# Kernel optimization log

Measured on AMD Instinct MI355X. Metric: run time of the kernel, lower is better.

Reference implementation:

```python
import jax, jax.numpy as jnp
import numpy as np

HIDDEN = 384
NDIM = 3
N_POINTS = 100000
N_SUPER = 2048
MAX_DEG = 32
RADIUS = 0.045
INPUT_DIM = 3


def _sincos_embed(coords):
    # ContinuousSincosEmbed: dim=384, ndim=3 -> 128 channels per spatial dim (64 sin + 64 cos)
    eff = HIDDEN // NDIM  # 128
    omega = jnp.arange(0, eff, 2, dtype=jnp.float32) / eff
    freq = 1.0 / (10000.0 ** omega)  # [eff//2]
    out = coords[..., None] * freq  # [..., ndim, eff//2]
    emb = jnp.concatenate([jnp.sin(out), jnp.cos(out)], axis=-1)  # [..., ndim, eff]
    return emb.reshape(coords.shape[:-1] + (HIDDEN,))


def _radius_neighbors(pos, sn_idx):
    # numpy preprocessing equivalent of torch_geometric.nn.pool.radius with
    # max_num_neighbors=MAX_DEG; fixed-size padded [S, K] output + validity mask.
    nbr = np.zeros((N_SUPER, MAX_DEG), np.int32)
    mask = np.zeros((N_SUPER, MAX_DEG), bool)
    pos2 = (pos ** 2).sum(-1)
    r2 = RADIUS * RADIUS
    chunk = 128
    for i0 in range(0, N_SUPER, chunk):
        sp = pos[sn_idx[i0:i0 + chunk]]
        d2 = (sp ** 2).sum(-1)[:, None] + pos2[None, :] - 2.0 * (sp @ pos.T)
        within = d2 <= r2
        for j in range(sp.shape[0]):
            idx = np.nonzero(within[j])[0][:MAX_DEG]
            nbr[i0 + j, :len(idx)] = idx
            mask[i0 + j, :len(idx)] = True
    return nbr, mask


def setup_inputs() -> dict:
    rng = np.random.default_rng(0)
    pos = rng.random((N_POINTS, NDIM)).astype(np.float32)
    sn_idx = np.sort(rng.choice(N_POINTS, N_SUPER, replace=False)).astype(np.int32)
    nbr, mask = _radius_neighbors(pos, sn_idx)
    key = jax.random.key(0)
    ks = jax.random.split(key, 6)
    s = 0.02  # truncnormal002 init scale
    return {
        "input_pos": jnp.asarray(pos),
        "input_feat": jax.random.normal(ks[0], (N_POINTS, INPUT_DIM), jnp.float32),
        "supernode_idx": jnp.asarray(sn_idx),
        "neighbor_idx": jnp.asarray(nbr),
        "neighbor_mask": jnp.asarray(mask),
        "W_in": jax.random.normal(ks[1], (INPUT_DIM, HIDDEN), jnp.float32) * s,
        "b_in": jnp.zeros((HIDDEN,), jnp.float32),
        "W1": jax.random.normal(ks[2], (2 * HIDDEN, HIDDEN), jnp.float32) * s,
        "b1": jnp.zeros((HIDDEN,), jnp.float32),
        "W2": jax.random.normal(ks[3], (HIDDEN, HIDDEN), jnp.float32) * s,
        "b2": jnp.zeros((HIDDEN,), jnp.float32),
        "W_proj": jax.random.normal(ks[4], (2 * HIDDEN, HIDDEN), jnp.float32) * s,
        "b_proj": jnp.zeros((HIDDEN,), jnp.float32),
    }


def reference(input_pos, input_feat, supernode_idx, neighbor_idx, neighbor_mask,
              W_in, b_in, W1, b1, W2, b2, W_proj, b_proj):
    # point embeddings: continuous sincos pos embed + input feature projection
    x = _sincos_embed(input_pos) + input_feat @ W_in + b_in          # [N, D]
    sn = x[supernode_idx]                                            # [S, D] supernode pos embed
    src = x[neighbor_idx]                                            # [S, K, D] gathered neighbors
    dst = jnp.broadcast_to(sn[:, None, :], src.shape)                # [S, K, D]
    h = jnp.concatenate([src, dst], axis=-1)                         # [S, K, 2D]
    # message MLP (Linear -> GELU(exact) -> Linear), as nn.GELU default
    h = jax.nn.gelu(h @ W1 + b1, approximate=False) @ W2 + b2        # [S, K, D]
    # masked mean == segment_csr(..., reduce='mean') over variable-degree edges
    m = neighbor_mask[..., None].astype(h.dtype)
    agg = (h * m).sum(axis=1) / jnp.maximum(m.sum(axis=1), 1.0)      # [S, D]
    # readd_supernode_pos: concat supernode pos embed, project 2D -> D
    out = jnp.concatenate([agg, sn], axis=-1) @ W_proj + b_proj      # [S, D]
    return out[None]                                                 # [1, S, D] (batch_size=1)
```

## Files before the change

### kernel.cpp

```cpp
#include <hip/hip_runtime.h>
#include <hip/hip_bf16.h>
#include <cstdint>

#define HIDDEN 384
#define NSUPER 2048
#define WBLK  (12*24*64*8)

typedef __attribute__((ext_vector_type(8)))  short bf16x8;
typedef __attribute__((ext_vector_type(4)))  float f32x4;
typedef __attribute__((ext_vector_type(16))) float f32x16;

__device__ inline unsigned short f2bf(float f) {
    unsigned int u = __float_as_uint(f);
    return (unsigned short)((u + 0x7fffu + ((u >> 16) & 1u)) >> 16);
}
__device__ inline bf16x8 pack8(const float* v) {
    union { bf16x8 v8; unsigned short u[8]; } u;
    #pragma unroll
    for (int i = 0; i < 8; ++i) u.u[i] = f2bf(v[i]);
    return u.v8;
}
__device__ inline float gelu(float y) {
    const float y2 = y * y;
    const float m  = __expf(y * fmaf(-0.0713548163f, y2, -1.5957691216f));
    return y * (1.0f / (1.0f + m));
}

__global__ __launch_bounds__(256)
void prep(const float* __restrict__ W1, const float* __restrict__ W2,
          const float* __restrict__ Wp, const unsigned int* __restrict__ mask,
          const float* __restrict__ pos, const float* __restrict__ feat,
          const int* __restrict__ sn_idx,
          const float* __restrict__ W_in, const float* __restrict__ b_in,
          unsigned short* __restrict__ w1s32, unsigned short* __restrict__ w1df,
          unsigned short* __restrict__ w2f,  unsigned short* __restrict__ wpf,
          unsigned short* __restrict__ snxb, int* __restrict__ flag) {
    const int b = blockIdx.x;
    const int t = threadIdx.x;
    if (b == 360) {
        __shared__ int s;
        if (t == 0) s = 0;
        __syncthreads();
        int bad = 0;
        for (int i = t; i < 16384; i += 256)
            if (mask[i] > 1u) bad = 1;
        if (bad) s = 1;
        __syncthreads();
        if (t == 0) *flag = s;
        return;
    }
    if (b > 360) {
        __shared__ float W4[HIDDEN][4];
        __shared__ float P6[64][7];
        const int eb = b - 361;
        if (t < 64) {
            const int pi = sn_idx[eb*64 + t];
            P6[t][0]=pos[pi*3];  P6[t][1]=pos[pi*3+1];  P6[t][2]=pos[pi*3+2];
            P6[t][3]=feat[pi*3]; P6[t][4]=feat[pi*3+1]; P6[t][5]=feat[pi*3+2];
        }
        for (int d = t; d < HIDDEN; d += 256) {
            W4[d][0]=W_in[d]; W4[d][1]=W_in[HIDDEN+d];
            W4[d][2]=W_in[2*HIDDEN+d]; W4[d][3]=b_in[d];
        }
        __syncthreads();
        const int er = t >> 2, seg = t & 3;
        float frA[8], frB[8];
        #pragma unroll
        for (int i = 0; i < 8; ++i) {
            frA[i] = exp2f(-(float)(seg*8 + i)      * 0.2076205059304601f);
            frB[i] = exp2f(-(float)(32 + seg*8 + i) * 0.2076205059304601f);
        }
        const float f0 = P6[er][3], f1 = P6[er][4], f2 = P6[er][5];
        #pragma unroll
        for (int cc = 0; cc < 3; ++cc) {
            const float pc = P6[er][cc];
            float sL[8], sH[8], cL[8], cH[8];
            #pragma unroll
            for (int i = 0; i < 8; ++i) {
                const float aL = pc*frA[i], aH = pc*frB[i];
                sL[i]=__sinf(aL); sH[i]=__sinf(aH); cL[i]=__cosf(aL); cH[i]=__cosf(aH);
            }
            #pragma unroll
            for (int q = 0; q < 4; ++q) {
                const float* bb = (q==0)?sL:(q==1)?sH:(q==2)?cL:cH;
                const int blk = cc*4 + q;
                float v[8];
                #pragma unroll
                for (int i = 0; i < 8; ++i) {
                    const int dim = blk*32 + seg*8 + i;
                    const float4 wv = *(const float4*)W4[dim];
                    v[i] = fmaf(f0, wv.x, fmaf(f1, wv.y, fmaf(f2, wv.z, bb[i] + wv.w)));
                }
                *(bf16x8*)&snxb[(size_t)(eb*64 + er)*HIDDEN + blk*32 + seg*8] = pack8(v);
            }
        }
        return;
    }
    const int grp = b / 72, sub = b % 72;
    const int idx = sub * 256 + t;
    const int l   = idx & 63;
    const int frag= idx >> 6;
    const float* W; unsigned short* out;
    int col, k0;
    if (grp == 0) {
        W = W1; out = w1s32;
        const int nt = frag % 12, kt = frag / 12;
        col = nt*32 + (l & 31);
        k0  = kt*16 + (l >> 5)*8;
    } else {
        switch (grp) {
            case 1: W = W1 + 384*HIDDEN; out = w1df; break;
            case 2: W = W2;              out = w2f;  break;
            case 3: W = Wp;              out = wpf;  break;
            default:W = Wp + 384*HIDDEN; out = wpf + WBLK; break;
        }
        const int nt = frag % 24, kt = frag / 24;
        col = nt*16 + (l & 15);
        k0  = kt*32 + (l >> 4)*8;
    }
    unsigned int pk[4];
    #pragma unroll
    for (int j = 0; j < 4; ++j) {
        unsigned int lo = f2bf(W[(size_t)(k0 + 2*j)     * HIDDEN + col]);
        unsigned int hi = f2bf(W[(size_t)(k0 + 2*j + 1) * HIDDEN + col]);
        pk[j] = lo | (hi << 16);
    }
    *reinterpret_cast<uint4*>(&out[(size_t)idx * 8]) =
        *reinterpret_cast<const uint4*>(pk);
}

__global__ __launch_bounds__(256)
void k_dstv(const unsigned short* __restrict__ snxb,
            const unsigned short* __restrict__ w1df,
            const float* __restrict__ b1, float* __restrict__ dstv) {
    const int rg = blockIdx.x >> 2, cq = blockIdx.x & 3;
    const int t = threadIdx.x, w = t>>6, l = t&63, lg = l>>4, l15 = l&15;
    const int wgm = w>>1, wgn = w&1;
    const int r0 = rg*64 + wgm*32;
    const int ntb = cq*6 + wgn*3;
    f32x4 acc[2][3];
    #pragma unroll
    for (int mt=0; mt<2; ++mt)
        #pragma unroll
        for (int nt=0; nt<3; ++nt) acc[mt][nt] = (f32x4){0.f,0.f,0.f,0.f};
    #pragma unroll 2
    for (int kt = 0; kt < 12; ++kt) {
        bf16x8 a[2], bfr[3];
        const unsigned short* bpp = &w1df[((size_t)(kt*24 + ntb)*64 + l)*8];
        #pragma unroll
        for (int nt=0; nt<3; ++nt) bfr[nt] = *(const bf16x8*)(bpp + (size_t)nt*512);
        #pragma unroll
        for (int mt=0; mt<2; ++mt)
            a[mt] = *(const bf16x8*)&snxb[(size_t)(r0 + mt*16 + l15)*HIDDEN + kt*32 + lg*8];
        #pragma unroll
        for (int mt=0; mt<2; ++mt)
            #pragma unroll
            for (int nt=0; nt<3; ++nt)
                acc[mt][nt] = __builtin_amdgcn_mfma_f32_16x16x32_bf16(a[mt], bfr[nt], acc[mt][nt], 0,0,0);
    }
    #pragma unroll
    for (int mt=0; mt<2; ++mt)
        #pragma unroll
        for (int nt=0; nt<3; ++nt) {
            const int col = cq*96 + wgn*48 + nt*16 + l15;
            #pragma unroll
            for (int r=0; r<4; ++r) {
                const int row = r0 + mt*16 + lg*4 + r;
                dstv[(size_t)row*HIDDEN + col] = acc[mt][nt][r] + b1[col];
            }
        }
}

__global__ __launch_bounds__(1024)
void k_mlp(const float* __restrict__ pos, const float* __restrict__ feat,
           const int* __restrict__ nbr_idx, const void* __restrict__ mask_raw,
           const int* __restrict__ mask_fmt,
           const float* __restrict__ W_in, const float* __restrict__ b_in,
           const float* __restrict__ dstv,
           const unsigned short* __restrict__ W1s32,
           unsigned short* __restrict__ aggpre, float* __restrict__ cntf)
{
    __shared__ unsigned short G[4*24*64*8];
    __shared__ float WIN0[HIDDEN], WIN1[HIDDEN], WIN2[HIDDEN], WINB[HIDDEN];
    __shared__ float PF[128][7];
    __shared__ float CNT[4];

    const int t  = threadIdx.x;
    const int bm = blockIdx.x;
    const int l = t & 63, w = t >> 6;
    const int mg = w >> 2, ng = w & 3;

    if (t < 128) {
        const int e  = bm*128 + t;
        const int pi = nbr_idx[e];
        PF[t][0]=pos[pi*3];  PF[t][1]=pos[pi*3+1];  PF[t][2]=pos[pi*3+2];
        PF[t][3]=feat[pi*3]; PF[t][4]=feat[pi*3+1]; PF[t][5]=feat[pi*3+2];
        const int fmt = *mask_fmt;
        const int mv  = fmt ? (int)((const unsigned char*)mask_raw)[e]
                            : ((const int*)mask_raw)[e];
        PF[t][6] = mv ? 1.0f : 0.0f;
    } else if (t >= 128 && t < 128 + HIDDEN) {
        const int d = t - 128;
        WIN0[d] = W_in[d];          WIN1[d] = W_in[HIDDEN + d];
        WIN2[d] = W_in[2*HIDDEN+d]; WINB[d] = b_in[d];
    }
    __syncthreads();
    if (t < 4) {
        float c = 0.f;
        for (int s = 0; s < 32; ++s) c += PF[t*32+s][6];
        CNT[t] = c;
    }

    {
        const int er = t >> 3, seg = t & 7;
        float frS[8];
        #pragma unroll
        for (int j = 0; j < 8; ++j)
            frS[j] = exp2f(-(float)(seg*8 + j) * 0.2076205059304601f);
        const float f0 = PF[er][3], f1 = PF[er][4], f2 = PF[er][5];
        const float pcs[3] = {PF[er][0], PF[er][1], PF[er][2]};
        const int lane = 32*(seg&1) + (er&31);
        const int ktb  = seg >> 1;
        const int mtb  = (er>>5)*24;
        #pragma unroll
        for (int cc = 0; cc < 3; ++cc) {
            const float pc = pcs[cc];
            #pragma unroll
            for (int sc = 0; sc < 2; ++sc) {
                const int kt = cc*8 + sc*4 + ktb;
                float v[8];
                #pragma unroll
                for (int j = 0; j < 8; ++j) {
                    const int dim = cc*128 + sc*64 + seg*8 + j;
                    const float aa = pc * frS[j];
                    const float base = sc ? __cosf(aa) : __sinf(aa);
                    v[j] = fmaf(f0, WIN0[dim], fmaf(f1, WIN1[dim],
                           fmaf(f2, WIN2[dim], base + WINB[dim])));
                }
                *(bf16x8*)&G[(size_t)((mtb + kt)*64 + lane)*8] = pack8(v);
            }
        }
    }
    __syncthreads();

    f32x16 acc[3];
    #pragma unroll
    for (int nt = 0; nt < 3; ++nt)
        #pragma unroll
        for (int r = 0; r < 16; ++r) acc[nt][r] = 0.f;

    bf16x8 bA[3], bB[3], aA, aB;
    #define LOADB(dst, kt)                                                       \
        { const unsigned short* bp_ = &W1s32[((size_t)((kt)*12 + ng*3)*64 + l)*8];\
          _Pragma("unroll")                                                      \
          for (int nt_ = 0; nt_ < 3; ++nt_)                                      \
              dst[nt_] = *(const bf16x8*)(bp_ + (size_t)nt_*512); }
    #define AREAD(kt) (*(const bf16x8*)&G[(size_t)((mg*24 + (kt))*64 + l)*8])
    #define MFMA3(bfr, a_)                                                       \
        { __builtin_amdgcn_s_setprio(1);                                         \
          _Pragma("unroll")                                                      \
          for (int nt_ = 0; nt_ < 3; ++nt_)                                      \
              acc[nt_] = __builtin_amdgcn_mfma_f32_32x32x16_bf16(                \
                  a_, bfr[nt_], acc[nt_], 0, 0, 0);                              \
          __builtin_amdgcn_s_setprio(0); }

    LOADB(bA, 0); LOADB(bB, 1);
    aA = AREAD(0); aB = AREAD(1);
    #pragma unroll
    for (int kt = 0; kt < 24; kt += 2) {
        MFMA3(bA, aA);
        if (kt + 2 < 24) { LOADB(bA, kt + 2); aA = AREAD(kt + 2); }
        MFMA3(bB, aB);
        if (kt + 3 < 24) { LOADB(bB, kt + 3); aB = AREAD(kt + 3); }
    }
    #undef LOADB
    #undef AREAD
    #undef MFMA3

    const int lh = l >> 5, l31 = l & 31;
    const int sn = bm*4 + mg;
    float dv[3];
    #pragma unroll
    for (int nt = 0; nt < 3; ++nt)
        dv[nt] = dstv[(size_t)sn*HIDDEN + ng*96 + nt*32 + l31];
    float mvr[16];
    #pragma unroll
    for (int r = 0; r < 16; ++r) {
        const int row = (r & 3) + 8*(r >> 2) + 4*lh;
        mvr[r] = PF[mg*32 + row][6];
    }
    const float inv = 1.0f / fmaxf(CNT[mg], 1.f);
    #pragma unroll
    for (int nt = 0; nt < 3; ++nt) {
        float s = 0.f;
        #pragma unroll
        for (int r = 0; r < 16; ++r)
            s += mvr[r] * gelu(acc[nt][r] + dv[nt]);
        s += __shfl_xor(s, 32);
        if (lh == 0)
            aggpre[(size_t)sn*HIDDEN + ng*96 + nt*32 + l31] = f2bf(s * inv);
    }
    if (t < 4) cntf[bm*4 + t] = CNT[t];
}

__global__ __launch_bounds__(256)
void k_out(const unsigned short* __restrict__ aggpre,
           const unsigned short* __restrict__ snxb,
           const unsigned short* __restrict__ w2f,
           const unsigned short* __restrict__ wpf,
           const float* __restrict__ b2, const float* __restrict__ bp,
           const float* __restrict__ cntf, float* __restrict__ out) {
    __shared__ unsigned short AGG[64][392];
    const int rg = blockIdx.x >> 2, cq = blockIdx.x & 3;
    const int t = threadIdx.x, w = t>>6, l = t&63, lg = l>>4, l15 = l&15;
    const int wgm = w>>1, wgn = w&1;
    const int r0g = rg*64;
    {
        const int rowm = wgm*32;
        f32x4 acc[2][12];
        #pragma unroll
        for (int mt=0; mt<2; ++mt)
            #pragma unroll
            for (int nt=0; nt<12; ++nt) acc[mt][nt] = (f32x4){0.f,0.f,0.f,0.f};
        for (int kt = 0; kt < 12; ++kt) {
            bf16x8 a[2], bfr[12];
            const unsigned short* bpp = &w2f[((size_t)(kt*24 + wgn*12)*64 + l)*8];
            #pragma unroll
            for (int nt=0; nt<12; ++nt) bfr[nt] = *(const bf16x8*)(bpp + (size_t)nt*512);
            #pragma unroll
            for (int mt=0; mt<2; ++mt)
                a[mt] = *(const bf16x8*)&aggpre[(size_t)(r0g + rowm + mt*16 + l15)*HIDDEN + kt*32 + lg*8];
            #pragma unroll
            for (int mt=0; mt<2; ++mt)
                #pragma unroll
                for (int nt=0; nt<12; ++nt)
                    acc[mt][nt] = __builtin_amdgcn_mfma_f32_16x16x32_bf16(a[mt], bfr[nt], acc[mt][nt], 0,0,0);
        }
        #pragma unroll
        for (int mt=0; mt<2; ++mt)
            #pragma unroll
            for (int nt=0; nt<12; ++nt) {
                const int col = wgn*192 + nt*16 + l15;
                const float bb = b2[col];
                #pragma unroll
                for (int r=0; r<4; ++r) {
                    const int row = rowm + mt*16 + lg*4 + r;
                    const float nz = (cntf[r0g + row] > 0.f) ? 1.f : 0.f;
                    AGG[row][col] = f2bf(acc[mt][nt][r] + bb*nz);
                }
            }
    }
    __syncthreads();
    const int r0 = r0g + wgm*32;
    const int ntb = cq*6 + wgn*3;
    f32x4 acc[2][3];
    #pragma unroll
    for (int mt=0; mt<2; ++mt)
        #pragma unroll
        for (int nt=0; nt<3; ++nt) acc[mt][nt] = (f32x4){0.f,0.f,0.f,0.f};
    #pragma unroll 2
    for (int kt = 0; kt < 24; ++kt) {
        const unsigned short* Wb = (kt < 12) ? wpf : wpf + WBLK;
        const int ktt = (kt < 12) ? kt : kt - 12;
        bf16x8 a[2], bfr[3];
        const unsigned short* bpp = &Wb[((size_t)(ktt*24 + ntb)*64 + l)*8];
        #pragma unroll
        for (int nt=0; nt<3; ++nt) bfr[nt] = *(const bf16x8*)(bpp + (size_t)nt*512);
        #pragma unroll
        for (int mt=0; mt<2; ++mt) {
            if (kt < 12)
                a[mt] = *(const bf16x8*)&AGG[wgm*32 + mt*16 + l15][ktt*32 + lg*8];
            else
                a[mt] = *(const bf16x8*)&snxb[(size_t)(r0 + mt*16 + l15)*HIDDEN + ktt*32 + lg*8];
        }
        #pragma unroll
        for (int mt=0; mt<2; ++mt)
            #pragma unroll
            for (int nt=0; nt<3; ++nt)
                acc[mt][nt] = __builtin_amdgcn_mfma_f32_16x16x32_bf16(a[mt], bfr[nt], acc[mt][nt], 0,0,0);
    }
    #pragma unroll
    for (int mt=0; mt<2; ++mt)
        #pragma unroll
        for (int nt=0; nt<3; ++nt) {
            const int col = cq*96 + wgn*48 + nt*16 + l15;
            #pragma unroll
            for (int r=0; r<4; ++r) {
                const int row = r0 + mt*16 + lg*4 + r;
                out[(size_t)row*HIDDEN + col] = acc[mt][nt][r] + bp[col];
            }
        }
}

extern "C" void kernel_launch(void* const* d_in, const int* in_sizes, int n_in,
                              void* d_out, int out_size, void* d_ws, size_t ws_size,
                              hipStream_t stream) {
    const float* pos   = (const float*)d_in[0];
    const float* feat  = (const float*)d_in[1];
    const int*   sn    = (const int*)d_in[2];
    const int*   nbr   = (const int*)d_in[3];
    const void*  mask  = d_in[4];
    const float* W_in  = (const float*)d_in[5];
    const float* b_in  = (const float*)d_in[6];
    const float* W1    = (const float*)d_in[7];
    const float* b1    = (const float*)d_in[8];
    const float* W2    = (const float*)d_in[9];
    const float* b2    = (const float*)d_in[10];
    const float* Wp    = (const float*)d_in[11];
    const float* bpv   = (const float*)d_in[12];
    float* out = (float*)d_out;

    char* base = (char*)d_ws;
    int* flag = (int*)base;
    unsigned short* w1s32 = (unsigned short*)(base + 256);
    unsigned short* w1df = w1s32 + WBLK;
    unsigned short* w2f  = w1df + WBLK;
    unsigned short* wpf  = w2f  + WBLK;
    unsigned short* snxb = wpf  + 2*(size_t)WBLK;
    unsigned short* aggp = snxb + (size_t)NSUPER*HIDDEN;
    float* cntf = (float*)(aggp + (size_t)NSUPER*HIDDEN);
    float* dstv = cntf + NSUPER;

    hipLaunchKernelGGL(prep, dim3(393), dim3(256), 0, stream,
                       W1, W2, Wp, (const unsigned int*)mask,
                       pos, feat, sn, W_in, b_in,
                       w1s32, w1df, w2f, wpf, snxb, flag);
    hipLaunchKernelGGL(k_dstv, dim3(128), dim3(256), 0, stream,
                       snxb, w1df, b1, dstv);
    hipLaunchKernelGGL(k_mlp, dim3(512), dim3(1024), 0, stream,
                       pos, feat, nbr, mask, flag, W_in, b_in, dstv,
                       w1s32, aggp, cntf);
    hipLaunchKernelGGL(k_out, dim3(128), dim3(256), 0, stream,
                       aggp, snxb, w2f, wpf, b2, bpv, cntf, out);
}
```

Before: 92.49 us.

## Warp-specialize k_mlp: producer waves embed halves while consumer waves run MFMA

Splits the 16 waves of k_mlp into 4 producer waves that build the bf16 sincos+projection embedding tile in two halves (double-buffered LDS), and 12 consumer waves that each own one 32-column N tile and run the W1 MFMA over two 32-row M tiles. The second half is embedded while the first half's GEMM runs, so embedding math overlaps with MFMA work. In exchange, only 4 waves now do all the embedding, so that phase is longer per half. Each consumer wave also loads its own B fragments for two M tiles, which changes register pressure and global-load reuse.

```diff
diff --git a/kernel.cpp b/kernel.cpp
--- a/kernel.cpp
+++ b/kernel.cpp
@@ -180,7 +180,7 @@
            const unsigned short* __restrict__ W1s32,
            unsigned short* __restrict__ aggpre, float* __restrict__ cntf)
 {
-    __shared__ unsigned short G[4*24*64*8];
+    __shared__ unsigned short G[2][2*24*64*8];
     __shared__ float WIN0[HIDDEN], WIN1[HIDDEN], WIN2[HIDDEN], WINB[HIDDEN];
     __shared__ float PF[128][7];
     __shared__ float CNT[4];
@@ -188,7 +188,6 @@
     const int t  = threadIdx.x;
     const int bm = blockIdx.x;
     const int l = t & 63, w = t >> 6;
-    const int mg = w >> 2, ng = w & 3;
 
     if (t < 128) {
         const int e  = bm*128 + t;
@@ -199,7 +198,7 @@
         const int mv  = fmt ? (int)((const unsigned char*)mask_raw)[e]
                             : ((const int*)mask_raw)[e];
         PF[t][6] = mv ? 1.0f : 0.0f;
-    } else if (t >= 128 && t < 128 + HIDDEN) {
+    } else if (t < 128 + HIDDEN) {
         const int d = t - 128;
         WIN0[d] = W_in[d];          WIN1[d] = W_in[HIDDEN + d];
         WIN2[d] = W_in[2*HIDDEN+d]; WINB[d] = b_in[d];
@@ -211,95 +210,97 @@
         CNT[t] = c;
     }
 
-    {
-        const int er = t >> 3, seg = t & 7;
-        float frS[8];
-        #pragma unroll
-        for (int j = 0; j < 8; ++j)
-            frS[j] = exp2f(-(float)(seg*8 + j) * 0.2076205059304601f);
-        const float f0 = PF[er][3], f1 = PF[er][4], f2 = PF[er][5];
-        const float pcs[3] = {PF[er][0], PF[er][1], PF[er][2]};
-        const int lane = 32*(seg&1) + (er&31);
-        const int ktb  = seg >> 1;
-        const int mtb  = (er>>5)*24;
-        #pragma unroll
-        for (int cc = 0; cc < 3; ++cc) {
-            const float pc = pcs[cc];
-            #pragma unroll
-            for (int sc = 0; sc < 2; ++sc) {
-                const int kt = cc*8 + sc*4 + ktb;
-                float v[8];
-                #pragma unroll
-                for (int j = 0; j < 8; ++j) {
-                    const int dim = cc*128 + sc*64 + seg*8 + j;
-                    const float aa = pc * frS[j];
-                    const float base = sc ? __cosf(aa) : __sinf(aa);
-                    v[j] = fmaf(f0, WIN0[dim], fmaf(f1, WIN1[dim],
-                           fmaf(f2, WIN2[dim], base + WINB[dim])));
-                }
-                *(bf16x8*)&G[(size_t)((mtb + kt)*64 + lane)*8] = pack8(v);
-            }
-        }
-    }
+    const int ew  = w - 12;
+    const int rl0 = ew*16 + (l & 15);
+    const int ec  = l >> 4;
+    float frL[8], frH[8];
+    #pragma unroll
+    for (int j = 0; j < 8; ++j) {
+        frL[j] = exp2f(-(float)(ec*8 + j)      * 0.2076205059304601f);
+        frH[j] = exp2f(-(float)(ec*8 + 32 + j) * 0.2076205059304601f);
+    }
+    auto embed_half = [&](int h, unsigned short* gb) {
+        const int row = h*64 + rl0;
+        const float f0 = PF[row][3], f1 = PF[row][4], f2 = PF[row][5];
+        const float pcs[3] = {PF[row][0], PF[row][1], PF[row][2]};
+        const int mt = rl0 >> 5, r31 = rl0 & 31;
+        const int ktc = ec >> 1, hi = ec & 1;
+        #pragma unroll
+        for (int m = 0; m < 12; ++m) {
+            const float pc = pcs[m>>2];
+            float v[8];
+            #pragma unroll
+            for (int j = 0; j < 8; ++j) {
+                const float fr = (m & 1) ? frH[j] : frL[j];
+                const float aa = pc * fr;
+                const float base = ((m>>1) & 1) ? __cosf(aa) : __sinf(aa);
+                const int dim = m*32 + ec*8 + j;
+                v[j] = fmaf(f0, WIN0[dim], fmaf(f1, WIN1[dim],
+                       fmaf(f2, WIN2[dim], base + WINB[dim])));
+            }
+            const int kt = 2*m + ktc;
+            *(bf16x8*)&gb[(size_t)((mt*24 + kt)*64 + 32*hi + r31)*8] = pack8(v);
+        }
+    };
+
+    const int nt = w;
+    const int lh = l >> 5, l31 = l & 31;
+    float dv[4] = {0.f, 0.f, 0.f, 0.f};
+    if (w < 12) {
+        #pragma unroll
+        for (int s = 0; s < 4; ++s)
+            dv[s] = dstv[(size_t)(bm*4 + s)*HIDDEN + nt*32 + l31];
+    }
+    auto gemm_half = [&](int h, const unsigned short* gb) {
+        f32x16 acc0, acc1;
+        #pragma unroll
+        for (int r = 0; r < 16; ++r) { acc0[r] = 0.f; acc1[r] = 0.f; }
+        bf16x8 bA = *(const bf16x8*)&W1s32[((size_t)(0*12 + nt)*64 + l)*8];
+        bf16x8 bB = *(const bf16x8*)&W1s32[((size_t)(1*12 + nt)*64 + l)*8];
+        #pragma unroll
+        for (int kt = 0; kt < 24; kt += 2) {
+            bf16x8 a0 = *(const bf16x8*)&gb[(size_t)(( 0 + kt)*64 + l)*8];
+            bf16x8 a1 = *(const bf16x8*)&gb[(size_t)((24 + kt)*64 + l)*8];
+            __builtin_amdgcn_s_setprio(1);
+            acc0 = __builtin_amdgcn_mfma_f32_32x32x16_bf16(a0, bA, acc0, 0,0,0);
+            acc1 = __builtin_amdgcn_mfma_f32_32x32x16_bf16(a1, bA, acc1, 0,0,0);
+            __builtin_amdgcn_s_setprio(0);
+            if (kt + 2 < 24)
+                bA = *(const bf16x8*)&W1s32[((size_t)((kt+2)*12 + nt)*64 + l)*8];
+            a0 = *(const bf16x8*)&gb[(size_t)(( 0 + kt+1)*64 + l)*8];
+            a1 = *(const bf16x8*)&gb[(size_t)((24 + kt+1)*64 + l)*8];
+            __builtin_amdgcn_s_setprio(1);
+            acc0 = __builtin_amdgcn_mfma_f32_32x32x16_bf16(a0, bB, acc0, 0,0,0);
+            acc1 = __builtin_amdgcn_mfma_f32_32x32x16_bf16(a1, bB, acc1, 0,0,0);
+            __builtin_amdgcn_s_setprio(0);
+            if (kt + 3 < 24)
+                bB = *(const bf16x8*)&W1s32[((size_t)((kt+3)*12 + nt)*64 + l)*8];
+        }
+        #pragma unroll
+        for (int mt = 0; mt < 2; ++mt) {
+            const f32x16 acc = mt ? acc1 : acc0;
+            const int sn    = bm*4 + h*2 + mt;
+            const float dvv = dv[h*2 + mt];
+            float s = 0.f;
+            #pragma unroll
+            for (int r = 0; r < 16; ++r) {
+                const int rr = (r & 3) + 8*(r >> 2) + 4*lh;
+                const float mv = PF[h*64 + mt*32 + rr][6];
+                s += mv * gelu(acc[r] + dvv);
+            }
+            s += __shfl_xor(s, 32);
+            if (lh == 0)
+                aggpre[(size_t)sn*HIDDEN + nt*32 + l31] =
+                    f2bf(s / fmaxf(CNT[h*2 + mt], 1.f));
+        }
+    };
+
+    if (w >= 12) embed_half(0, G[0]);
     __syncthreads();
-
-    f32x16 acc[3];
-    #pragma unroll
-    for (int nt = 0; nt < 3; ++nt)
-        #pragma unroll
-        for (int r = 0; r < 16; ++r) acc[nt][r] = 0.f;
-
-    bf16x8 bA[3], bB[3], aA, aB;
-    #define LOADB(dst, kt)                                                       \
-        { const unsigned short* bp_ = &W1s32[((size_t)((kt)*12 + ng*3)*64 + l)*8];\
-          _Pragma("unroll")                                                      \
-          for (int nt_ = 0; nt_ < 3; ++nt_)                                      \
-              dst[nt_] = *(const bf16x8*)(bp_ + (size_t)nt_*512); }
-    #define AREAD(kt) (*(const bf16x8*)&G[(size_t)((mg*24 + (kt))*64 + l)*8])
-    #define MFMA3(bfr, a_)                                                       \
-        { __builtin_amdgcn_s_setprio(1);                                         \
-          _Pragma("unroll")                                                      \
-          for (int nt_ = 0; nt_ < 3; ++nt_)                                      \
-              acc[nt_] = __builtin_amdgcn_mfma_f32_32x32x16_bf16(                \
-                  a_, bfr[nt_], acc[nt_], 0, 0, 0);                              \
-          __builtin_amdgcn_s_setprio(0); }
-
-    LOADB(bA, 0); LOADB(bB, 1);
-    aA = AREAD(0); aB = AREAD(1);
-    #pragma unroll
-    for (int kt = 0; kt < 24; kt += 2) {
-        MFMA3(bA, aA);
-        if (kt + 2 < 24) { LOADB(bA, kt + 2); aA = AREAD(kt + 2); }
-        MFMA3(bB, aB);
-        if (kt + 3 < 24) { LOADB(bB, kt + 3); aB = AREAD(kt + 3); }
-    }
-    #undef LOADB
-    #undef AREAD
-    #undef MFMA3
-
-    const int lh = l >> 5, l31 = l & 31;
-    const int sn = bm*4 + mg;
-    float dv[3];
-    #pragma unroll
-    for (int nt = 0; nt < 3; ++nt)
-        dv[nt] = dstv[(size_t)sn*HIDDEN + ng*96 + nt*32 + l31];
-    float mvr[16];
-    #pragma unroll
-    for (int r = 0; r < 16; ++r) {
-        const int row = (r & 3) + 8*(r >> 2) + 4*lh;
-        mvr[r] = PF[mg*32 + row][6];
-    }
-    const float inv = 1.0f / fmaxf(CNT[mg], 1.f);
-    #pragma unroll
-    for (int nt = 0; nt < 3; ++nt) {
-        float s = 0.f;
-        #pragma unroll
-        for (int r = 0; r < 16; ++r)
-            s += mvr[r] * gelu(acc[nt][r] + dv[nt]);
-        s += __shfl_xor(s, 32);
-        if (lh == 0)
-            aggpre[(size_t)sn*HIDDEN + ng*96 + nt*32 + l31] = f2bf(s * inv);
-    }
+    if (w >= 12) embed_half(1, G[1]);
+    else         gemm_half(0, G[0]);
+    __syncthreads();
+    if (w < 12)  gemm_half(1, G[1]);
     if (t < 4) cntf[bm*4 + t] = CNT[t];
 }
 
```

New measurement: 90.56 us. 1.02x faster.
